# Performance work log

Measured on AMD Instinct MI355X. Metric: run time of the kernel, lower is better.

## Reference

```python
import jax, jax.numpy as jnp
import numpy as np

EPS = 1e-6
NUM_HEADS = 4


def setup_inputs() -> dict:
    key = jax.random.key(0)
    ks = jax.random.split(key, 7)
    B, C, H, W = 4, 128, 64, 64
    x = jax.random.normal(ks[0], (B, C, H, W), dtype=jnp.float32)
    norm_w = jnp.ones((C,), dtype=jnp.float32)
    norm_b = jnp.zeros((C,), dtype=jnp.float32)
    # 1x1 convs stored as [out_ch, in_ch] matrices
    qkv_w = jax.random.normal(ks[1], (3 * C, C), dtype=jnp.float32) / np.sqrt(C)
    qkv_b = jnp.zeros((3 * C,), dtype=jnp.float32)
    proj_w = jax.random.normal(ks[2], (C, C), dtype=jnp.float32) / np.sqrt(C)
    proj_b = jnp.zeros((C,), dtype=jnp.float32)
    return {"x": x, "norm_w": norm_w, "norm_b": norm_b,
            "qkv_w": qkv_w, "qkv_b": qkv_b, "proj_w": proj_w, "proj_b": proj_b}


def reference(x, norm_w, norm_b, qkv_w, qkv_b, proj_w, proj_b):
    B, C, H, W = x.shape
    nh = NUM_HEADS
    dh = C // nh
    N = H * W

    # ChannelLayerNorm: stats over channel dim per spatial position
    mean = jnp.mean(x, axis=1, keepdims=True)
    var = jnp.mean(jnp.square(x - mean), axis=1, keepdims=True)  # unbiased=False
    h = (x - mean) * jax.lax.rsqrt(var + EPS)
    h = h * norm_w[None, :, None, None] + norm_b[None, :, None, None]

    # qkv 1x1 conv -> [B, 3C, H, W]
    qkv = jnp.einsum('oc,bchw->bohw', qkv_w, h) + qkv_b[None, :, None, None]
    qkv = qkv.reshape(B, 3, nh, dh, N)
    q, k, v = qkv[:, 0], qkv[:, 1], qkv[:, 2]  # each [B, nh, dh, N]

    scale = dh ** -0.5
    attn = jnp.einsum('bhcn,bhcm->bhnm', q, k) * scale  # [B, nh, N, N]
    attn = jax.nn.softmax(attn, axis=-1)
    h = jnp.einsum('bhnm,bhcm->bhcn', attn, v)  # [B, nh, dh, N]
    h = h.reshape(B, C, H, W)

    h = jnp.einsum('oc,bchw->bohw', proj_w, h) + proj_b[None, :, None, None]
    return x + h
```

## Files before the change

kernel.cpp:

```cpp
#include <hip/hip_runtime.h>
#include <hip/hip_bf16.h>
#include <math.h>

#define BB 4
#define CC 128
#define NH 4
#define DH 32
#define NN 4096
#define OC3 (3*CC)

typedef __attribute__((ext_vector_type(8))) short short8;
typedef __attribute__((ext_vector_type(4))) short short4v;
typedef __attribute__((ext_vector_type(4))) float float4v;

__device__ inline short f2bf(float f) {
    unsigned u = __builtin_bit_cast(unsigned, f);
    u += 0x7FFF + ((u >> 16) & 1);
    return (short)(u >> 16);
}
__device__ inline unsigned pk2bf(float a, float b) {
    __hip_bfloat162 h = __float22bfloat162_rn(make_float2(a, b));
    unsigned u; __builtin_memcpy(&u, &h, 4);
    return u;
}

__global__ __launch_bounds__(256) void wcvt_kernel(
        const float* __restrict__ qw, const float* __restrict__ pw,
        short* __restrict__ wb) {
    int i = (blockIdx.x * 256 + threadIdx.x) * 8;
    const float* src = (i < OC3 * CC) ? (qw + i) : (pw + (i - OC3 * CC));
    float4 f0 = *(const float4*)(src);
    float4 f1 = *(const float4*)(src + 4);
    union { short8 v; unsigned u[4]; } z;
    z.u[0] = pk2bf(f0.x, f0.y); z.u[1] = pk2bf(f0.z, f0.w);
    z.u[2] = pk2bf(f1.x, f1.y); z.u[3] = pk2bf(f1.z, f1.w);
    *(short8*)(wb + i) = z.v;
}

#define HS 136
__global__ __launch_bounds__(512, 4) void lnqkv_kernel(
        const float* __restrict__ x, const float* __restrict__ nw,
        const float* __restrict__ nb, const short* __restrict__ qwb,
        const float* __restrict__ qbias,
        short* __restrict__ qT, short* __restrict__ kT, short* __restrict__ vv) {
    __shared__ short hT[64 * HS];
    __shared__ float red[16][64];
    __shared__ float mrs[2][64];
    int t = threadIdx.x;
    int n0g = blockIdx.x * 64;
    int b = n0g >> 12, n0 = n0g & (NN - 1);
    int nl = t & 63, cq = t >> 6;

    const float* xp = x + ((size_t)b * CC + cq * 16) * NN + n0 + nl;
    float xv[16];
    float s = 0.f, ss = 0.f;
    #pragma unroll
    for (int j = 0; j < 16; ++j) {
        xv[j] = xp[(size_t)j * NN];
        s += xv[j]; ss += xv[j] * xv[j];
    }
    red[cq][nl] = s; red[cq + 8][nl] = ss;
    __syncthreads();
    if (t < 64) {
        float s8 = 0.f, q8 = 0.f;
        #pragma unroll
        for (int j = 0; j < 8; ++j) { s8 += red[j][t]; q8 += red[j + 8][t]; }
        float mean = s8 * (1.0f / CC);
        float var  = q8 * (1.0f / CC) - mean * mean;
        mrs[0][t] = mean;
        mrs[1][t] = rsqrtf(var + 1e-6f);
    }
    __syncthreads();
    {
        float mean = mrs[0][nl], rsv = mrs[1][nl];
        #pragma unroll
        for (int j = 0; j < 16; j += 8) {
            union { short8 v; unsigned u[4]; } z;
            #pragma unroll
            for (int k = 0; k < 4; ++k) {
                int c = cq * 16 + j + 2 * k;
                float h0 = (xv[j + 2 * k]     - mean) * rsv * nw[c]     + nb[c];
                float h1 = (xv[j + 2 * k + 1] - mean) * rsv * nw[c + 1] + nb[c + 1];
                z.u[k] = pk2bf(h0, h1);
            }
            *(short8*)&hT[nl * HS + cq * 16 + j] = z.v;
        }
    }
    __syncthreads();

    int w = t >> 6, lane = t & 63;
    int lg = lane >> 4, ln = lane & 15;
    #pragma unroll
    for (int it = 0; it < 3; ++it) {
        int ow = (w + it * 8) * 16;
        const short* wp = qwb + (size_t)(ow + ln) * CC;
        float4v a0 = {0,0,0,0}, a1 = {0,0,0,0}, a2 = {0,0,0,0}, a3 = {0,0,0,0};
        #pragma unroll
        for (int cs = 0; cs < 4; ++cs) {
            short8 af = *(const short8*)(wp + cs * 32 + lg * 8);
            const short* hp = &hT[cs * 32 + lg * 8];
            a0 = __builtin_amdgcn_mfma_f32_16x16x32_bf16(af, *(const short8*)&hp[(0  + ln) * HS], a0, 0, 0, 0);
            a1 = __builtin_amdgcn_mfma_f32_16x16x32_bf16(af, *(const short8*)&hp[(16 + ln) * HS], a1, 0, 0, 0);
            a2 = __builtin_amdgcn_mfma_f32_16x16x32_bf16(af, *(const short8*)&hp[(32 + ln) * HS], a2, 0, 0, 0);
            a3 = __builtin_amdgcn_mfma_f32_16x16x32_bf16(af, *(const short8*)&hp[(48 + ln) * HS], a3, 0, 0, 0);
        }
        int r0 = ow + lg * 4;
        float b0 = qbias[r0], b1 = qbias[r0 + 1], b2 = qbias[r0 + 2], b3 = qbias[r0 + 3];
        int cb = ow & 31;
        float4v* accs[4] = {&a0, &a1, &a2, &a3};
        if (it == 0) {
            const float qs = 0.1767766952966369f * 1.4426950408889634f;
            int hh = ow >> 5;
            size_t rowbase = (size_t)(b * NH + hh) * NN + n0;
            #pragma unroll
            for (int nsub = 0; nsub < 4; ++nsub) {
                float4v av = *accs[nsub];
                union { short4v v; unsigned u[2]; } z;
                z.u[0] = pk2bf((av.x + b0) * qs, (av.y + b1) * qs);
                z.u[1] = pk2bf((av.z + b2) * qs, (av.w + b3) * qs);
                *(short4v*)&qT[(rowbase + nsub * 16 + ln) * DH + cb + lg * 4] = z.v;
            }
        } else if (it == 1) {
            int hh = (ow - CC) >> 5;
            size_t rowbase = (size_t)(b * NH + hh) * NN + n0;
            #pragma unroll
            for (int nsub = 0; nsub < 4; ++nsub) {
                float4v av = *accs[nsub];
                union { short4v v; unsigned u[2]; } z;
                z.u[0] = pk2bf(av.x + b0, av.y + b1);
                z.u[1] = pk2bf(av.z + b2, av.w + b3);
                *(short4v*)&kT[(rowbase + nsub * 16 + ln) * DH + cb + lg * 4] = z.v;
            }
        } else {
            int hh = (ow - 2 * CC) >> 5;
            size_t cbase = (size_t)((b * NH + hh) * DH + cb + lg * 4);
            #pragma unroll
            for (int nsub = 0; nsub < 4; ++nsub) {
                float4v av = *accs[nsub];
                size_t col = (size_t)n0 + nsub * 16 + ln;
                vv[(cbase + 0) * NN + col] = f2bf(av.x + b0);
                vv[(cbase + 1) * NN + col] = f2bf(av.y + b1);
                vv[(cbase + 2) * NN + col] = f2bf(av.z + b2);
                vv[(cbase + 3) * NN + col] = f2bf(av.w + b3);
            }
        }
    }
}

#define PS 72
union __align__(16) FlashSh {
    short pt[8 * 16 * PS];
    struct { float mo[3][8][64][8]; float ml[3][8][64]; } m;
};
__global__ __launch_bounds__(512, 2) void flash_kernel(
        const short* __restrict__ qT, const short* __restrict__ kT,
        const short* __restrict__ vv, short* __restrict__ aoT) {
    __shared__ FlashSh sh;
    int blk = blockIdx.x;
    int bh = blk >> 5;
    int qb = blk & 31;
    int b = bh >> 2, hh = bh & 3;
    int n0 = qb * 128;
    int t = threadIdx.x, w = t >> 6, lane = t & 63;
    int lg = lane >> 4, ln = lane & 15;
    int qg = w & 1;
    int split = w >> 1;

    const short* kbase = kT + (size_t)bh * NN * DH + lg * 8;
    const short* vb0 = vv + ((size_t)bh * DH + ln) * NN + lg * 8;
    const short* vb1 = vb0 + (size_t)16 * NN;

    short8 qf[4];
    #pragma unroll
    for (int j = 0; j < 4; ++j)
        qf[j] = *(const short8*)&qT[((size_t)bh * NN + n0 + (qg * 4 + j) * 16 + ln) * DH + lg * 8];

    union { short8 v; unsigned u[4]; } onesf;
    onesf.u[0] = 0x3F803F80u; onesf.u[1] = 0x3F803F80u;
    onesf.u[2] = 0x3F803F80u; onesf.u[3] = 0x3F803F80u;

    float4v o0[4], o1[4], sacc[4];
    #pragma unroll
    for (int j = 0; j < 4; ++j) {
        o0[j] = (float4v){0,0,0,0}; o1[j] = (float4v){0,0,0,0};
        sacc[j] = (float4v){0,0,0,0};
    }
    short* ptw = &sh.pt[w * 16 * PS];

    int mbeg = split * (NN / 4), mend = mbeg + NN / 4;
    for (int m0 = mbeg; m0 < mend; m0 += 64) {
        const short* kp = kbase + (size_t)m0 * DH;
        short8 k0 = *(const short8*)(kp + (size_t)(ln +  0) * DH);
        short8 k1 = *(const short8*)(kp + (size_t)(ln + 16) * DH);
        short8 k2 = *(const short8*)(kp + (size_t)(ln + 32) * DH);
        short8 k3 = *(const short8*)(kp + (size_t)(ln + 48) * DH);
        short8 v0 = *(const short8*)(vb0 + m0);
        short8 v1 = *(const short8*)(vb0 + m0 + 32);
        short8 v2 = *(const short8*)(vb1 + m0);
        short8 v3 = *(const short8*)(vb1 + m0 + 32);

        #pragma unroll
        for (int j = 0; j < 4; ++j) {
            float4v s0 = {0,0,0,0}, s1 = s0, s2 = s0, s3 = s0;
            s0 = __builtin_amdgcn_mfma_f32_16x16x32_bf16(k0, qf[j], s0, 0, 0, 0);
            s1 = __builtin_amdgcn_mfma_f32_16x16x32_bf16(k1, qf[j], s1, 0, 0, 0);
            s2 = __builtin_amdgcn_mfma_f32_16x16x32_bf16(k2, qf[j], s2, 0, 0, 0);
            s3 = __builtin_amdgcn_mfma_f32_16x16x32_bf16(k3, qf[j], s3, 0, 0, 0);
            float4v* sv[4] = {&s0, &s1, &s2, &s3};
            #pragma unroll
            for (int jj = 0; jj < 4; ++jj) {
                float4v sj = *sv[jj];
                float p0 = __builtin_amdgcn_exp2f(sj.x);
                float p1 = __builtin_amdgcn_exp2f(sj.y);
                float p2 = __builtin_amdgcn_exp2f(sj.z);
                float p3 = __builtin_amdgcn_exp2f(sj.w);
                union { short4v v; unsigned u[2]; } z;
                z.u[0] = pk2bf(p0, p1); z.u[1] = pk2bf(p2, p3);
                *(short4v*)&ptw[ln * PS + jj * 16 + lg * 4] = z.v;
            }
            short8 pb0 = *(const short8*)&ptw[ln * PS + 0  + lg * 8];
            short8 pb1 = *(const short8*)&ptw[ln * PS + 32 + lg * 8];
            o0[j]   = __builtin_amdgcn_mfma_f32_16x16x32_bf16(v0, pb0, o0[j], 0, 0, 0);
            o1[j]   = __builtin_amdgcn_mfma_f32_16x16x32_bf16(v2, pb0, o1[j], 0, 0, 0);
            sacc[j] = __builtin_amdgcn_mfma_f32_16x16x32_bf16(onesf.v, pb0, sacc[j], 0, 0, 0);
            o0[j]   = __builtin_amdgcn_mfma_f32_16x16x32_bf16(v1, pb1, o0[j], 0, 0, 0);
            o1[j]   = __builtin_amdgcn_mfma_f32_16x16x32_bf16(v3, pb1, o1[j], 0, 0, 0);
            sacc[j] = __builtin_amdgcn_mfma_f32_16x16x32_bf16(onesf.v, pb1, sacc[j], 0, 0, 0);
        }
    }

    float ls[4];
    #pragma unroll
    for (int j = 0; j < 4; ++j) ls[j] = sacc[j].x;

    __syncthreads();
    if (split > 0) {
        int si = split - 1;
        #pragma unroll
        for (int j = 0; j < 4; ++j) {
            int tid = qg * 4 + j;
            float* mp = &sh.m.mo[si][tid][lane][0];
            *(float4*)(mp + 0) = make_float4(o0[j].x, o0[j].y, o0[j].z, o0[j].w);
            *(float4*)(mp + 4) = make_float4(o1[j].x, o1[j].y, o1[j].z, o1[j].w);
            sh.m.ml[si][tid][lane] = ls[j];
        }
    }
    __syncthreads();
    if (split == 0) {
        #pragma unroll
        for (int j = 0; j < 4; ++j) {
            int tid = qg * 4 + j;
            #pragma unroll
            for (int si = 0; si < 3; ++si) {
                const float* mp = &sh.m.mo[si][tid][lane][0];
                float4 a0 = *(const float4*)(mp + 0);
                float4 a1 = *(const float4*)(mp + 4);
                o0[j].x += a0.x; o0[j].y += a0.y; o0[j].z += a0.z; o0[j].w += a0.w;
                o1[j].x += a1.x; o1[j].y += a1.y; o1[j].z += a1.z; o1[j].w += a1.w;
                ls[j] += sh.m.ml[si][tid][lane];
            }
            float inv = 1.0f / ls[j];
            short* ap = aoT + ((size_t)b * NN + n0 + tid * 16 + ln) * CC + hh * DH;
            union { short4v v; unsigned u[2]; } z;
            z.u[0] = pk2bf(o0[j].x * inv, o0[j].y * inv);
            z.u[1] = pk2bf(o0[j].z * inv, o0[j].w * inv);
            *(short4v*)&ap[lg * 4] = z.v;
            z.u[0] = pk2bf(o1[j].x * inv, o1[j].y * inv);
            z.u[1] = pk2bf(o1[j].z * inv, o1[j].w * inv);
            *(short4v*)&ap[16 + lg * 4] = z.v;
        }
    }
}

__global__ __launch_bounds__(256) void proj_kernel(
        const short* __restrict__ aoT, const short* __restrict__ pwb,
        const float* __restrict__ pb, const float* __restrict__ x,
        float* __restrict__ out) {
    int t = threadIdx.x;
    int n0g = blockIdx.x * 64;
    int b = n0g >> 12, n0 = n0g & (NN - 1);
    int o0 = blockIdx.y * 64;
    int wo = t >> 6, lane = t & 63;
    int lg = lane >> 4, ln = lane & 15;
    int ow = o0 + wo * 16;
    const short* wp = pwb + (size_t)(ow + ln) * CC;
    const short* ap = aoT + (size_t)n0g * CC + lg * 8;
    float4v a0 = {0,0,0,0}, a1 = {0,0,0,0}, a2 = {0,0,0,0}, a3 = {0,0,0,0};
    #pragma unroll
    for (int cs = 0; cs < 4; ++cs) {
        short8 af = *(const short8*)(wp + cs * 32 + lg * 8);
        const short* hp = ap + cs * 32;
        a0 = __builtin_amdgcn_mfma_f32_16x16x32_bf16(af, *(const short8*)&hp[(size_t)(0  + ln) * CC], a0, 0, 0, 0);
        a1 = __builtin_amdgcn_mfma_f32_16x16x32_bf16(af, *(const short8*)&hp[(size_t)(16 + ln) * CC], a1, 0, 0, 0);
        a2 = __builtin_amdgcn_mfma_f32_16x16x32_bf16(af, *(const short8*)&hp[(size_t)(32 + ln) * CC], a2, 0, 0, 0);
        a3 = __builtin_amdgcn_mfma_f32_16x16x32_bf16(af, *(const short8*)&hp[(size_t)(48 + ln) * CC], a3, 0, 0, 0);
    }
    int r0 = ow + lg * 4;
    float b0 = pb[r0], b1 = pb[r0 + 1], b2 = pb[r0 + 2], b3 = pb[r0 + 3];
    const float* xbase = x   + ((size_t)b * CC + r0) * NN + n0 + ln;
    float*       obase = out + ((size_t)b * CC + r0) * NN + n0 + ln;
    float4v* accs[4] = {&a0, &a1, &a2, &a3};
    #pragma unroll
    for (int nsub = 0; nsub < 4; ++nsub) {
        float4v av = *accs[nsub];
        const float* xp = xbase + nsub * 16;
        float* op = obase + nsub * 16;
        op[(size_t)0 * NN] = av.x + b0 + xp[(size_t)0 * NN];
        op[(size_t)1 * NN] = av.y + b1 + xp[(size_t)1 * NN];
        op[(size_t)2 * NN] = av.z + b2 + xp[(size_t)2 * NN];
        op[(size_t)3 * NN] = av.w + b3 + xp[(size_t)3 * NN];
    }
}

extern "C" void kernel_launch(void* const* d_in, const int* in_sizes, int n_in,
                              void* d_out, int out_size, void* d_ws, size_t ws_size,
                              hipStream_t stream) {
    const float* x    = (const float*)d_in[0];
    const float* nw   = (const float*)d_in[1];
    const float* nb   = (const float*)d_in[2];
    const float* qkvw = (const float*)d_in[3];
    const float* qkvb = (const float*)d_in[4];
    const float* pw   = (const float*)d_in[5];
    const float* pb   = (const float*)d_in[6];
    float* out = (float*)d_out;

    short* qT  = (short*)d_ws;
    short* kT  = qT + (size_t)BB * NH * NN * DH;
    short* vv  = kT + (size_t)BB * NH * NN * DH;
    short* aoT = vv + (size_t)BB * NH * DH * NN;
    short* wb  = aoT + (size_t)BB * NH * DH * NN;
    short* qwb = wb;
    short* pwb = wb + (size_t)OC3 * CC;

    wcvt_kernel<<<dim3(32), 256, 0, stream>>>(qkvw, pw, wb);
    lnqkv_kernel<<<dim3(256), 512, 0, stream>>>(x, nw, nb, qwb, qkvb, qT, kT, vv);
    flash_kernel<<<dim3(512), 512, 0, stream>>>(qT, kT, vv, aoT);
    proj_kernel<<<dim3(256, 2), 256, 0, stream>>>(aoT, pwb, pb, x, out);
}
```

Baseline: 153.5 us.

## Split flash attention over 8 key ranges with tree reduction and VALU row sums

Each block now handles 64 queries instead of 128, and all 8 waves share the same queries while each covers its own eighth of the keys. The grid doubles to 1024 blocks. The row-sum MFMA against a ones vector is replaced by VALU adds plus cross-lane shuffles, which removes a third of the PV-stage MFMAs. Partial results are merged with a 3-level tree reduction through shared memory using padded rows. The trade-off is twice the K/V global traffic per query, more syncthreads, and more reduction work.

```diff
diff --git a/kernel.cpp b/kernel.cpp
--- a/kernel.cpp
+++ b/kernel.cpp
@@ -150,21 +150,20 @@
 #define PS 72
 union __align__(16) FlashSh {
     short pt[8 * 16 * PS];
-    struct { float mo[3][8][64][8]; float ml[3][8][64]; } m;
+    float m[4][4][64][10];
 };
 __global__ __launch_bounds__(512, 2) void flash_kernel(
         const short* __restrict__ qT, const short* __restrict__ kT,
         const short* __restrict__ vv, short* __restrict__ aoT) {
     __shared__ FlashSh sh;
     int blk = blockIdx.x;
-    int bh = blk >> 5;
-    int qb = blk & 31;
+    int bh = blk >> 6;
+    int qb = blk & 63;
     int b = bh >> 2, hh = bh & 3;
-    int n0 = qb * 128;
+    int n0 = qb * 64;
     int t = threadIdx.x, w = t >> 6, lane = t & 63;
     int lg = lane >> 4, ln = lane & 15;
-    int qg = w & 1;
-    int split = w >> 1;
+    int split = w;
 
     const short* kbase = kT + (size_t)bh * NN * DH + lg * 8;
     const short* vb0 = vv + ((size_t)bh * DH + ln) * NN + lg * 8;
@@ -173,21 +172,17 @@
     short8 qf[4];
     #pragma unroll
     for (int j = 0; j < 4; ++j)
-        qf[j] = *(const short8*)&qT[((size_t)bh * NN + n0 + (qg * 4 + j) * 16 + ln) * DH + lg * 8];
-
-    union { short8 v; unsigned u[4]; } onesf;
-    onesf.u[0] = 0x3F803F80u; onesf.u[1] = 0x3F803F80u;
-    onesf.u[2] = 0x3F803F80u; onesf.u[3] = 0x3F803F80u;
-
-    float4v o0[4], o1[4], sacc[4];
+        qf[j] = *(const short8*)&qT[((size_t)bh * NN + n0 + j * 16 + ln) * DH + lg * 8];
+
+    float4v o0[4], o1[4];
+    float ls[4];
     #pragma unroll
     for (int j = 0; j < 4; ++j) {
-        o0[j] = (float4v){0,0,0,0}; o1[j] = (float4v){0,0,0,0};
-        sacc[j] = (float4v){0,0,0,0};
+        o0[j] = (float4v){0,0,0,0}; o1[j] = (float4v){0,0,0,0}; ls[j] = 0.f;
     }
     short* ptw = &sh.pt[w * 16 * PS];
 
-    int mbeg = split * (NN / 4), mend = mbeg + NN / 4;
+    int mbeg = split * (NN / 8), mend = mbeg + NN / 8;
     for (int m0 = mbeg; m0 < mend; m0 += 64) {
         const short* kp = kbase + (size_t)m0 * DH;
         short8 k0 = *(const short8*)(kp + (size_t)(ln +  0) * DH);
@@ -206,6 +201,7 @@
             s1 = __builtin_amdgcn_mfma_f32_16x16x32_bf16(k1, qf[j], s1, 0, 0, 0);
             s2 = __builtin_amdgcn_mfma_f32_16x16x32_bf16(k2, qf[j], s2, 0, 0, 0);
             s3 = __builtin_amdgcn_mfma_f32_16x16x32_bf16(k3, qf[j], s3, 0, 0, 0);
+            float lacc = 0.f;
             float4v* sv[4] = {&s0, &s1, &s2, &s3};
             #pragma unroll
             for (int jj = 0; jj < 4; ++jj) {
@@ -214,60 +210,116 @@
                 float p1 = __builtin_amdgcn_exp2f(sj.y);
                 float p2 = __builtin_amdgcn_exp2f(sj.z);
                 float p3 = __builtin_amdgcn_exp2f(sj.w);
+                lacc += (p0 + p1) + (p2 + p3);
                 union { short4v v; unsigned u[2]; } z;
                 z.u[0] = pk2bf(p0, p1); z.u[1] = pk2bf(p2, p3);
                 *(short4v*)&ptw[ln * PS + jj * 16 + lg * 4] = z.v;
             }
+            ls[j] += lacc;
             short8 pb0 = *(const short8*)&ptw[ln * PS + 0  + lg * 8];
             short8 pb1 = *(const short8*)&ptw[ln * PS + 32 + lg * 8];
-            o0[j]   = __builtin_amdgcn_mfma_f32_16x16x32_bf16(v0, pb0, o0[j], 0, 0, 0);
-            o1[j]   = __builtin_amdgcn_mfma_f32_16x16x32_bf16(v2, pb0, o1[j], 0, 0, 0);
-            sacc[j] = __builtin_amdgcn_mfma_f32_16x16x32_bf16(onesf.v, pb0, sacc[j], 0, 0, 0);
-            o0[j]   = __builtin_amdgcn_mfma_f32_16x16x32_bf16(v1, pb1, o0[j], 0, 0, 0);
-            o1[j]   = __builtin_amdgcn_mfma_f32_16x16x32_bf16(v3, pb1, o1[j], 0, 0, 0);
-            sacc[j] = __builtin_amdgcn_mfma_f32_16x16x32_bf16(onesf.v, pb1, sacc[j], 0, 0, 0);
-        }
-    }
-
-    float ls[4];
-    #pragma unroll
-    for (int j = 0; j < 4; ++j) ls[j] = sacc[j].x;
+            o0[j] = __builtin_amdgcn_mfma_f32_16x16x32_bf16(v0, pb0, o0[j], 0, 0, 0);
+            o1[j] = __builtin_amdgcn_mfma_f32_16x16x32_bf16(v2, pb0, o1[j], 0, 0, 0);
+            o0[j] = __builtin_amdgcn_mfma_f32_16x16x32_bf16(v1, pb1, o0[j], 0, 0, 0);
+            o1[j] = __builtin_amdgcn_mfma_f32_16x16x32_bf16(v3, pb1, o1[j], 0, 0, 0);
+        }
+    }
 
     __syncthreads();
-    if (split > 0) {
-        int si = split - 1;
-        #pragma unroll
-        for (int j = 0; j < 4; ++j) {
-            int tid = qg * 4 + j;
-            float* mp = &sh.m.mo[si][tid][lane][0];
-            *(float4*)(mp + 0) = make_float4(o0[j].x, o0[j].y, o0[j].z, o0[j].w);
-            *(float4*)(mp + 4) = make_float4(o1[j].x, o1[j].y, o1[j].z, o1[j].w);
-            sh.m.ml[si][tid][lane] = ls[j];
-        }
-    }
-    __syncthreads();
-    if (split == 0) {
-        #pragma unroll
-        for (int j = 0; j < 4; ++j) {
-            int tid = qg * 4 + j;
-            #pragma unroll
-            for (int si = 0; si < 3; ++si) {
-                const float* mp = &sh.m.mo[si][tid][lane][0];
-                float4 a0 = *(const float4*)(mp + 0);
-                float4 a1 = *(const float4*)(mp + 4);
-                o0[j].x += a0.x; o0[j].y += a0.y; o0[j].z += a0.z; o0[j].w += a0.w;
-                o1[j].x += a1.x; o1[j].y += a1.y; o1[j].z += a1.z; o1[j].w += a1.w;
-                ls[j] += sh.m.ml[si][tid][lane];
-            }
-            float inv = 1.0f / ls[j];
-            short* ap = aoT + ((size_t)b * NN + n0 + tid * 16 + ln) * CC + hh * DH;
-            union { short4v v; unsigned u[2]; } z;
-            z.u[0] = pk2bf(o0[j].x * inv, o0[j].y * inv);
-            z.u[1] = pk2bf(o0[j].z * inv, o0[j].w * inv);
-            *(short4v*)&ap[lg * 4] = z.v;
-            z.u[0] = pk2bf(o1[j].x * inv, o1[j].y * inv);
-            z.u[1] = pk2bf(o1[j].z * inv, o1[j].w * inv);
-            *(short4v*)&ap[16 + lg * 4] = z.v;
+    {
+        if (split & 1) {
+            int slot = split >> 1;
+            #pragma unroll
+            for (int j = 0; j < 4; ++j) {
+                float* mp = &sh.m[slot][j][lane][0];
+                *(float2*)(mp + 0) = make_float2(o0[j].x, o0[j].y);
+                *(float2*)(mp + 2) = make_float2(o0[j].z, o0[j].w);
+                *(float2*)(mp + 4) = make_float2(o1[j].x, o1[j].y);
+                *(float2*)(mp + 6) = make_float2(o1[j].z, o1[j].w);
+                mp[8] = ls[j];
+            }
+        }
+        __syncthreads();
+        if (!(split & 1)) {
+            int slot = split >> 1;
+            #pragma unroll
+            for (int j = 0; j < 4; ++j) {
+                const float* mp = &sh.m[slot][j][lane][0];
+                float2 a0 = *(const float2*)(mp + 0);
+                float2 a1 = *(const float2*)(mp + 2);
+                float2 a2 = *(const float2*)(mp + 4);
+                float2 a3 = *(const float2*)(mp + 6);
+                o0[j].x += a0.x; o0[j].y += a0.y; o0[j].z += a1.x; o0[j].w += a1.y;
+                o1[j].x += a2.x; o1[j].y += a2.y; o1[j].z += a3.x; o1[j].w += a3.y;
+                ls[j] += mp[8];
+            }
+        }
+        __syncthreads();
+        if ((split & 3) == 2) {
+            int slot = split >> 2;
+            #pragma unroll
+            for (int j = 0; j < 4; ++j) {
+                float* mp = &sh.m[slot][j][lane][0];
+                *(float2*)(mp + 0) = make_float2(o0[j].x, o0[j].y);
+                *(float2*)(mp + 2) = make_float2(o0[j].z, o0[j].w);
+                *(float2*)(mp + 4) = make_float2(o1[j].x, o1[j].y);
+                *(float2*)(mp + 6) = make_float2(o1[j].z, o1[j].w);
+                mp[8] = ls[j];
+            }
+        }
+        __syncthreads();
+        if ((split & 3) == 0) {
+            int slot = split >> 2;
+            #pragma unroll
+            for (int j = 0; j < 4; ++j) {
+                const float* mp = &sh.m[slot][j][lane][0];
+                float2 a0 = *(const float2*)(mp + 0);
+                float2 a1 = *(const float2*)(mp + 2);
+                float2 a2 = *(const float2*)(mp + 4);
+                float2 a3 = *(const float2*)(mp + 6);
+                o0[j].x += a0.x; o0[j].y += a0.y; o0[j].z += a1.x; o0[j].w += a1.y;
+                o1[j].x += a2.x; o1[j].y += a2.y; o1[j].z += a3.x; o1[j].w += a3.y;
+                ls[j] += mp[8];
+            }
+        }
+        __syncthreads();
+        if (split == 4) {
+            #pragma unroll
+            for (int j = 0; j < 4; ++j) {
+                float* mp = &sh.m[0][j][lane][0];
+                *(float2*)(mp + 0) = make_float2(o0[j].x, o0[j].y);
+                *(float2*)(mp + 2) = make_float2(o0[j].z, o0[j].w);
+                *(float2*)(mp + 4) = make_float2(o1[j].x, o1[j].y);
+                *(float2*)(mp + 6) = make_float2(o1[j].z, o1[j].w);
+                mp[8] = ls[j];
+            }
+        }
+        __syncthreads();
+        if (split == 0) {
+            #pragma unroll
+            for (int j = 0; j < 4; ++j) {
+                const float* mp = &sh.m[0][j][lane][0];
+                float2 a0 = *(const float2*)(mp + 0);
+                float2 a1 = *(const float2*)(mp + 2);
+                float2 a2 = *(const float2*)(mp + 4);
+                float2 a3 = *(const float2*)(mp + 6);
+                o0[j].x += a0.x; o0[j].y += a0.y; o0[j].z += a1.x; o0[j].w += a1.y;
+                o1[j].x += a2.x; o1[j].y += a2.y; o1[j].z += a3.x; o1[j].w += a3.y;
+                ls[j] += mp[8];
+
+                float lt = ls[j];
+                lt += __shfl_xor(lt, 16, 64);
+                lt += __shfl_xor(lt, 32, 64);
+                float inv = 1.0f / lt;
+                short* ap = aoT + ((size_t)b * NN + n0 + j * 16 + ln) * CC + hh * DH;
+                union { short4v v; unsigned u[2]; } z;
+                z.u[0] = pk2bf(o0[j].x * inv, o0[j].y * inv);
+                z.u[1] = pk2bf(o0[j].z * inv, o0[j].w * inv);
+                *(short4v*)&ap[lg * 4] = z.v;
+                z.u[0] = pk2bf(o1[j].x * inv, o1[j].y * inv);
+                z.u[1] = pk2bf(o1[j].z * inv, o1[j].w * inv);
+                *(short4v*)&ap[16 + lg * 4] = z.v;
+            }
         }
     }
 }
@@ -334,6 +386,6 @@
 
     wcvt_kernel<<<dim3(32), 256, 0, stream>>>(qkvw, pw, wb);
     lnqkv_kernel<<<dim3(256), 512, 0, stream>>>(x, nw, nb, qwb, qkvb, qT, kT, vv);
-    flash_kernel<<<dim3(512), 512, 0, stream>>>(qT, kT, vv, aoT);
+    flash_kernel<<<dim3(1024), 512, 0, stream>>>(qT, kT, vv, aoT);
     proj_kernel<<<dim3(256, 2), 256, 0, stream>>>(aoT, pwb, pb, x, out);
 }
```

Measured after the change: 157.7 us. 2.7% more time.
